# Kernel optimization log

Measured on AMD Instinct MI355X. Metric: run time of the kernel, lower is better.

Reference implementation:

```python
import jax, jax.numpy as jnp
import numpy as np

N_NODES = 200000  # num_users + num_items
N_EDGES = 1000000
D = 64


def setup_inputs() -> dict:
    key = jax.random.key(0)
    ks = jax.random.split(key, 9)
    return {
        "src": jax.random.randint(ks[0], (N_EDGES,), 0, N_NODES, dtype=jnp.int32),
        "dst": jax.random.randint(ks[1], (N_EDGES,), 0, N_NODES, dtype=jnp.int32),
        "review_feat": jax.random.normal(ks[2], (N_EDGES, D), dtype=jnp.float32),
        "ci_r": jax.random.uniform(ks[3], (N_NODES, 1), dtype=jnp.float32),
        "feature": jax.random.normal(ks[4], (N_NODES, D), dtype=jnp.float32),
        "W1": jax.random.normal(ks[5], (D, D), dtype=jnp.float32) * 0.05,
        "W2": jax.random.normal(ks[6], (D, D), dtype=jnp.float32) * 0.05,
        "feature2": jax.random.normal(ks[7], (N_NODES, D), dtype=jnp.float32) * 0.05,
        "feature3": jax.random.normal(ks[8], (N_NODES, D), dtype=jnp.float32) * 0.05,
    }


def reference(src, dst, review_feat, ci_r, feature, W1, W2, feature2, feature3):
    # Eval-mode forward (is_training=False, freeze='', dropout = identity).
    # `feature` is assigned to g.srcdata['h_r'] in the original but never used.
    n = ci_r.shape[0]
    ci_src = ci_r[src]            # [E,1] gather of src norm coeff
    ci_dst = ci_r                 # [N,1]

    # Pass 1: edge linear on review features, scaled by src coeff, scatter-sum.
    r = review_feat @ W1.T                                   # [E,64]
    h1 = jax.ops.segment_sum(r * ci_src, dst, num_segments=n)
    rst_re = h1 * ci_dst

    # Pass 2: (src embedding + edge transform) messages.
    r_fe = review_feat @ W2.T                                # [E,64]
    m2 = (feature2[src] + r_fe) * ci_src
    h2 = jax.ops.segment_sum(m2, dst, num_segments=n)
    rst = h2 * ci_dst

    # Pass 3: pure src-embedding messages.
    m3 = feature3[src] * ci_src
    h3 = jax.ops.segment_sum(m3, dst, num_segments=n)
    rst_id = h3 * ci_dst

    return (rst, rst_re, rst_id)
```

## Files before the change

kernel.cpp:

```cpp
#include <hip/hip_runtime.h>

#define NN 200000
#define NE 1000000
#define DD 64
#define NCHUNK 196

typedef __bf16 bf16x4 __attribute__((ext_vector_type(4)));
typedef __bf16 bf16x8 __attribute__((ext_vector_type(8)));
typedef float  f32x4  __attribute__((ext_vector_type(4)));

static __device__ __forceinline__ bf16x8 pack8(const float* __restrict__ p) {
    float4 a = *reinterpret_cast<const float4*>(p);
    float4 b = *reinterpret_cast<const float4*>(p + 4);
    bf16x8 r;
    r[0] = (__bf16)a.x; r[1] = (__bf16)a.y; r[2] = (__bf16)a.z; r[3] = (__bf16)a.w;
    r[4] = (__bf16)b.x; r[5] = (__bf16)b.y; r[6] = (__bf16)b.z; r[7] = (__bf16)b.w;
    return r;
}

__global__ __launch_bounds__(256) void k_zero(int* __restrict__ counts) {
    const int i = (blockIdx.x * 256 + threadIdx.x) * 4;
    if (i + 3 < NN) *reinterpret_cast<int4*>(counts + i) = make_int4(0, 0, 0, 0);
    else for (int j = i; j < NN; ++j) counts[j] = 0;
}

__global__ __launch_bounds__(256) void k_hist(const int* __restrict__ dst,
                                              int* __restrict__ counts) {
    for (int e = blockIdx.x * blockDim.x + threadIdx.x; e < NE;
         e += gridDim.x * blockDim.x)
        atomicAdd(&counts[dst[e]], 1);
}

__global__ __launch_bounds__(256) void k_chunk_sums(const int* __restrict__ counts,
                                                    int* __restrict__ csum) {
    const int b = blockIdx.x, tid = threadIdx.x;
    const int base = b * 1024 + tid * 4;
    int s = 0;
#pragma unroll
    for (int j = 0; j < 4; ++j) {
        const int i = base + j;
        if (i < NN) s += counts[i];
    }
#pragma unroll
    for (int d = 32; d > 0; d >>= 1) s += __shfl_down(s, d);
    __shared__ int wsum[4];
    if ((tid & 63) == 0) wsum[tid >> 6] = s;
    __syncthreads();
    if (tid == 0) csum[b] = wsum[0] + wsum[1] + wsum[2] + wsum[3];
}

__global__ void k_scan_chunks(const int* __restrict__ csum, int* __restrict__ cofs) {
    if (threadIdx.x == 0 && blockIdx.x == 0) {
        int acc = 0;
        for (int i = 0; i < NCHUNK; ++i) { cofs[i] = acc; acc += csum[i]; }
    }
}

__global__ __launch_bounds__(256) void k_chunk_scan(const int* __restrict__ counts,
                                                    const int* __restrict__ cofs,
                                                    int* __restrict__ offs,
                                                    int* __restrict__ cursor) {
    const int b = blockIdx.x, tid = threadIdx.x;
    const int lane = tid & 63, wv = tid >> 6;
    const int base = b * 1024 + tid * 4;
    int c[4];
#pragma unroll
    for (int j = 0; j < 4; ++j) {
        const int i = base + j;
        c[j] = (i < NN) ? counts[i] : 0;
    }
    const int ls = c[0] + c[1] + c[2] + c[3];
    int v = ls;
#pragma unroll
    for (int d = 1; d < 64; d <<= 1) {
        const int u = __shfl_up(v, d);
        if (lane >= d) v += u;
    }
    __shared__ int wsum[4];
    if (lane == 63) wsum[wv] = v;
    __syncthreads();
    int wbase = 0;
    for (int w = 0; w < wv; ++w) wbase += wsum[w];
    int excl = cofs[b] + wbase + (v - ls);
#pragma unroll
    for (int j = 0; j < 4; ++j) {
        const int i = base + j;
        if (i < NN) { offs[i] = excl; cursor[i] = excl; }
        excl += c[j];
    }
}

__global__ __launch_bounds__(256) void k_permfill(const int* __restrict__ dst,
                                                  const int* __restrict__ src,
                                                  const float* __restrict__ ci,
                                                  int* __restrict__ cursor,
                                                  int4* __restrict__ epack) {
    for (int e = blockIdx.x * blockDim.x + threadIdx.x; e < NE;
         e += gridDim.x * blockDim.x) {
        const int s = src[e];
        const float cs = ci[s];
        const int pos = atomicAdd(&cursor[dst[e]], 1);
        epack[pos] = make_int4(e, s, __float_as_int(cs), 0);
    }
}

__global__ __launch_bounds__(256) void k_pull_fused(
    const int4* __restrict__ epack, const int* __restrict__ offs,
    const int* __restrict__ counts, const float* __restrict__ review,
    const float* __restrict__ ci,
    const float* __restrict__ f2, const float* __restrict__ f3,
    const float* __restrict__ W1, const float* __restrict__ W2,
    float* __restrict__ out_rst, float* __restrict__ out_re,
    float* __restrict__ out_id)
{
    __shared__ __bf16 At[16][72];
    __shared__ float  S2[16][68];

    const int tid = threadIdx.x;
    const int l16 = tid & 15;
    const int q   = tid >> 4;
    const int n   = blockIdx.x * 16 + q;

    const int beg = offs[n];
    const int cnt = counts[n];

    float4 ax0 = {0,0,0,0}, a20 = {0,0,0,0}, a30 = {0,0,0,0};
    float4 ax1 = {0,0,0,0}, a21 = {0,0,0,0}, a31 = {0,0,0,0};

    int k = 0;
    for (; k + 2 <= cnt; k += 2) {
        const int4 ea = epack[beg + k];
        const int4 eb = epack[beg + k + 1];
        const float ca = __int_as_float(ea.z);
        const float cb = __int_as_float(eb.z);
        const float4 ra  = *reinterpret_cast<const float4*>(review + (size_t)ea.x * DD + l16 * 4);
        const float4 rb  = *reinterpret_cast<const float4*>(review + (size_t)eb.x * DD + l16 * 4);
        const float4 p2a = *reinterpret_cast<const float4*>(f2 + (size_t)ea.y * DD + l16 * 4);
        const float4 p2b = *reinterpret_cast<const float4*>(f2 + (size_t)eb.y * DD + l16 * 4);
        const float4 p3a = *reinterpret_cast<const float4*>(f3 + (size_t)ea.y * DD + l16 * 4);
        const float4 p3b = *reinterpret_cast<const float4*>(f3 + (size_t)eb.y * DD + l16 * 4);
        ax0.x = fmaf(ra.x, ca, ax0.x); ax0.y = fmaf(ra.y, ca, ax0.y);
        ax0.z = fmaf(ra.z, ca, ax0.z); ax0.w = fmaf(ra.w, ca, ax0.w);
        ax1.x = fmaf(rb.x, cb, ax1.x); ax1.y = fmaf(rb.y, cb, ax1.y);
        ax1.z = fmaf(rb.z, cb, ax1.z); ax1.w = fmaf(rb.w, cb, ax1.w);
        a20.x = fmaf(p2a.x, ca, a20.x); a20.y = fmaf(p2a.y, ca, a20.y);
        a20.z = fmaf(p2a.z, ca, a20.z); a20.w = fmaf(p2a.w, ca, a20.w);
        a21.x = fmaf(p2b.x, cb, a21.x); a21.y = fmaf(p2b.y, cb, a21.y);
        a21.z = fmaf(p2b.z, cb, a21.z); a21.w = fmaf(p2b.w, cb, a21.w);
        a30.x = fmaf(p3a.x, ca, a30.x); a30.y = fmaf(p3a.y, ca, a30.y);
        a30.z = fmaf(p3a.z, ca, a30.z); a30.w = fmaf(p3a.w, ca, a30.w);
        a31.x = fmaf(p3b.x, cb, a31.x); a31.y = fmaf(p3b.y, cb, a31.y);
        a31.z = fmaf(p3b.z, cb, a31.z); a31.w = fmaf(p3b.w, cb, a31.w);
    }
    if (k < cnt) {
        const int4 ea = epack[beg + k];
        const float ca = __int_as_float(ea.z);
        const float4 ra  = *reinterpret_cast<const float4*>(review + (size_t)ea.x * DD + l16 * 4);
        const float4 p2a = *reinterpret_cast<const float4*>(f2 + (size_t)ea.y * DD + l16 * 4);
        const float4 p3a = *reinterpret_cast<const float4*>(f3 + (size_t)ea.y * DD + l16 * 4);
        ax0.x = fmaf(ra.x, ca, ax0.x); ax0.y = fmaf(ra.y, ca, ax0.y);
        ax0.z = fmaf(ra.z, ca, ax0.z); ax0.w = fmaf(ra.w, ca, ax0.w);
        a20.x = fmaf(p2a.x, ca, a20.x); a20.y = fmaf(p2a.y, ca, a20.y);
        a20.z = fmaf(p2a.z, ca, a20.z); a20.w = fmaf(p2a.w, ca, a20.w);
        a30.x = fmaf(p3a.x, ca, a30.x); a30.y = fmaf(p3a.y, ca, a30.y);
        a30.z = fmaf(p3a.z, ca, a30.z); a30.w = fmaf(p3a.w, ca, a30.w);
    }

    const float cid = ci[n];
    float4 ax = {ax0.x + ax1.x, ax0.y + ax1.y, ax0.z + ax1.z, ax0.w + ax1.w};
    float4 a2 = {a20.x + a21.x, a20.y + a21.y, a20.z + a21.z, a20.w + a21.w};
    float4 a3 = {a30.x + a31.x, a30.y + a31.y, a30.z + a31.z, a30.w + a31.w};

    f32x4 v3 = {a3.x * cid, a3.y * cid, a3.z * cid, a3.w * cid};
    __builtin_nontemporal_store(v3, reinterpret_cast<f32x4*>(out_id + (size_t)n * DD + l16 * 4));

    bf16x4 hb;
    hb[0] = (__bf16)(ax.x * cid); hb[1] = (__bf16)(ax.y * cid);
    hb[2] = (__bf16)(ax.z * cid); hb[3] = (__bf16)(ax.w * cid);
    *reinterpret_cast<bf16x4*>(&At[q][l16 * 4]) = hb;
    float4 s2v = {a2.x * cid, a2.y * cid, a2.z * cid, a2.w * cid};
    *reinterpret_cast<float4*>(&S2[q][l16 * 4]) = s2v;
    __syncthreads();

    const int w  = tid >> 6;
    const int lq = (tid & 63) >> 4;
    bf16x8 w1f[2], w2f[2];
#pragma unroll
    for (int kk = 0; kk < 2; ++kk) {
        const int off = (w * 16 + l16) * DD + kk * 32 + lq * 8;
        w1f[kk] = pack8(W1 + off);
        w2f[kk] = pack8(W2 + off);
    }
    const bf16x8 a0 = *reinterpret_cast<const bf16x8*>(&At[l16][lq * 8]);
    const bf16x8 a1 = *reinterpret_cast<const bf16x8*>(&At[l16][lq * 8 + 32]);

    const f32x4 zero = {0.f, 0.f, 0.f, 0.f};
    f32x4 acc1 = zero, acc2 = zero;
    acc1 = __builtin_amdgcn_mfma_f32_16x16x32_bf16(a0, w1f[0], acc1, 0, 0, 0);
    acc1 = __builtin_amdgcn_mfma_f32_16x16x32_bf16(a1, w1f[1], acc1, 0, 0, 0);
    acc2 = __builtin_amdgcn_mfma_f32_16x16x32_bf16(a0, w2f[0], acc2, 0, 0, 0);
    acc2 = __builtin_amdgcn_mfma_f32_16x16x32_bf16(a1, w2f[1], acc2, 0, 0, 0);

    const int base = blockIdx.x * 16;
#pragma unroll
    for (int i = 0; i < 4; ++i) {
        const int row = lq * 4 + i;
        const size_t o = (size_t)(base + row) * DD + w * 16 + l16;
        __builtin_nontemporal_store(acc1[i], out_re + o);
        __builtin_nontemporal_store(acc2[i] + S2[row][w * 16 + l16], out_rst + o);
    }
}

__global__ __launch_bounds__(256) void gcn_mfma_kernel(
    const int* __restrict__ src, const int* __restrict__ dst,
    const float* __restrict__ review, const float* __restrict__ ci,
    const float* __restrict__ W1, const float* __restrict__ W2,
    const float* __restrict__ f2, const float* __restrict__ f3,
    float* __restrict__ out)
{
    float* out_rst = out;
    float* out_re  = out + (size_t)NN * DD;
    float* out_id  = out + 2 * (size_t)NN * DD;
    const int lane = threadIdx.x & 63;
    const int l16  = lane & 15;
    const int lq   = lane >> 4;
    const int wid  = blockIdx.x * (blockDim.x >> 6) + (threadIdx.x >> 6);
    const int nw   = gridDim.x * (blockDim.x >> 6);

    bf16x8 w1f[4][2], w2f[4][2];
#pragma unroll
    for (int c = 0; c < 4; ++c)
#pragma unroll
        for (int kk = 0; kk < 2; ++kk) {
            const int off = (c * 16 + l16) * DD + kk * 32 + lq * 8;
            w1f[c][kk] = pack8(W1 + off);
            w2f[c][kk] = pack8(W2 + off);
        }
    const f32x4 zero = {0.f, 0.f, 0.f, 0.f};
    for (int t = wid; t < NE / 16; t += nw) {
        const int e0 = t * 16;
        const float* xr = review + (size_t)(e0 + l16) * DD + lq * 8;
        const bf16x8 a0 = pack8(xr);
        const bf16x8 a1 = pack8(xr + 32);
        f32x4 acc1[4], acc2[4];
#pragma unroll
        for (int c = 0; c < 4; ++c) { acc1[c] = zero; acc2[c] = zero; }
#pragma unroll
        for (int c = 0; c < 4; ++c) {
            acc1[c] = __builtin_amdgcn_mfma_f32_16x16x32_bf16(a0, w1f[c][0], acc1[c], 0, 0, 0);
            acc1[c] = __builtin_amdgcn_mfma_f32_16x16x32_bf16(a1, w1f[c][1], acc1[c], 0, 0, 0);
            acc2[c] = __builtin_amdgcn_mfma_f32_16x16x32_bf16(a0, w2f[c][0], acc2[c], 0, 0, 0);
            acc2[c] = __builtin_amdgcn_mfma_f32_16x16x32_bf16(a1, w2f[c][1], acc2[c], 0, 0, 0);
        }
        int sA[4], dA[4]; float cf[4];
#pragma unroll
        for (int i = 0; i < 4; ++i) {
            const int e = e0 + lq * 4 + i;
            sA[i] = src[e]; dA[i] = dst[e];
            cf[i] = ci[sA[i]] * ci[dA[i]];
        }
#pragma unroll
        for (int i = 0; i < 4; ++i) {
            const size_t so = (size_t)sA[i] * DD;
            const size_t dofs = (size_t)dA[i] * DD;
            const float c_ = cf[i];
#pragma unroll
            for (int c = 0; c < 4; ++c) {
                const int col = c * 16 + l16;
                atomicAdd(out_re  + dofs + col, acc1[c][i] * c_);
                atomicAdd(out_rst + dofs + col, (f2[so + col] + acc2[c][i]) * c_);
                atomicAdd(out_id  + dofs + col, f3[so + col] * c_);
            }
        }
    }
}

extern "C" void kernel_launch(void* const* d_in, const int* in_sizes, int n_in,
                              void* d_out, int out_size, void* d_ws, size_t ws_size,
                              hipStream_t stream) {
    const int*   src    = (const int*)d_in[0];
    const int*   dst    = (const int*)d_in[1];
    const float* review = (const float*)d_in[2];
    const float* ci     = (const float*)d_in[3];
    const float* W1     = (const float*)d_in[5];
    const float* W2     = (const float*)d_in[6];
    const float* f2     = (const float*)d_in[7];
    const float* f3     = (const float*)d_in[8];
    float* out = (float*)d_out;
    float* out_rst = out;
    float* out_re  = out + (size_t)NN * DD;
    float* out_id  = out + 2 * (size_t)NN * DD;

    const size_t NEED = sizeof(int) * ((size_t)3 * NN + 512) +
                        sizeof(int4) * (size_t)NE;
    if (ws_size < NEED) {
        (void)hipMemsetAsync(out, 0, (size_t)out_size * sizeof(float), stream);
        gcn_mfma_kernel<<<2048, 256, 0, stream>>>(src, dst, review, ci, W1, W2, f2, f3, out);
        return;
    }

    char* w = (char*)d_ws;
    int* counts = (int*)w;    w += (size_t)NN * 4;
    int* offs   = (int*)w;    w += (size_t)NN * 4;
    int* cursor = (int*)w;    w += (size_t)NN * 4;
    int* csum   = (int*)w;    w += 256 * 4;
    int* cofs   = (int*)w;    w += 256 * 4;
    int4* epack = (int4*)w;

    k_zero        <<<(NN / 4 + 255) / 256, 256, 0, stream>>>(counts);
    k_hist        <<<1024, 256, 0, stream>>>(dst, counts);
    k_chunk_sums  <<<NCHUNK, 256, 0, stream>>>(counts, csum);
    k_scan_chunks <<<1, 64, 0, stream>>>(csum, cofs);
    k_chunk_scan  <<<NCHUNK, 256, 0, stream>>>(counts, cofs, offs, cursor);
    k_permfill    <<<1024, 256, 0, stream>>>(dst, src, ci, cursor, epack);
    k_pull_fused  <<<NN / 16, 256, 0, stream>>>(epack, offs, counts, review, ci,
                                                f2, f3, W1, W2,
                                                out_rst, out_re, out_id);
}
```

Before: 295.8 us.

## Pre-scale feature2/feature3 into packed bf16 table and pull per-wave node groups

Adds a conversion pass, co-scheduled with the edge permutation fill in one launch, that writes feature2 and feature3 pre-multiplied by ci as one interleaved bf16 row per node. The pull kernel then gathers a single 256-byte bf16 row per edge instead of two fp32 rows, roughly halving gather traffic for those tables. It also reorganises work so each 16-lane group walks a contiguous CSR range of 4 nodes, using offs[n+1] instead of counts, and each wave runs its own MFMA projection without a block barrier. The cost is the extra conversion pass, added workspace, and bf16 rounding of the src features and of the pass-2/3 messages, plus serial per-edge loads with only one-edge prefetch.

```diff
diff --git a/kernel.cpp b/kernel.cpp
--- a/kernel.cpp
+++ b/kernel.cpp
@@ -63,6 +63,7 @@
     const int b = blockIdx.x, tid = threadIdx.x;
     const int lane = tid & 63, wv = tid >> 6;
     const int base = b * 1024 + tid * 4;
+    if (b == 0 && tid == 0) offs[NN] = NE;
     int c[4];
 #pragma unroll
     for (int j = 0; j < 4; ++j) {
@@ -90,124 +91,131 @@
     }
 }
 
-__global__ __launch_bounds__(256) void k_permfill(const int* __restrict__ dst,
-                                                  const int* __restrict__ src,
-                                                  const float* __restrict__ ci,
-                                                  int* __restrict__ cursor,
-                                                  int4* __restrict__ epack) {
-    for (int e = blockIdx.x * blockDim.x + threadIdx.x; e < NE;
-         e += gridDim.x * blockDim.x) {
-        const int s = src[e];
-        const float cs = ci[s];
-        const int pos = atomicAdd(&cursor[dst[e]], 1);
-        epack[pos] = make_int4(e, s, __float_as_int(cs), 0);
-    }
-}
-
-__global__ __launch_bounds__(256) void k_pull_fused(
+__global__ __launch_bounds__(256) void k_fill_conv(
+    const int* __restrict__ dst, const int* __restrict__ src,
+    const float* __restrict__ ci, const float* __restrict__ f2,
+    const float* __restrict__ f3, int* __restrict__ cursor,
+    int4* __restrict__ epack, __bf16* __restrict__ ftc)
+{
+    const int b = blockIdx.x;
+    if (b < 1024) {
+        for (int e = b * 256 + threadIdx.x; e < NE; e += 1024 * 256) {
+            const int s = src[e];
+            const float cs = ci[s];
+            const int pos = atomicAdd(&cursor[dst[e]], 1);
+            epack[pos] = make_int4(e, s, __float_as_int(cs), 0);
+        }
+    } else {
+        const int nconv = (gridDim.x - 1024) * 256;
+        const int total = NN * 16;
+        for (int cch = (b - 1024) * 256 + threadIdx.x; cch < total; cch += nconv) {
+            const int row = cch >> 4;
+            const int t   = cch & 15;
+            const float c = ci[row];
+            const float4 a = *reinterpret_cast<const float4*>(f2 + (size_t)row * DD + t * 4);
+            const float4 v = *reinterpret_cast<const float4*>(f3 + (size_t)row * DD + t * 4);
+            bf16x8 o;
+            o[0] = (__bf16)(a.x * c); o[1] = (__bf16)(a.y * c);
+            o[2] = (__bf16)(a.z * c); o[3] = (__bf16)(a.w * c);
+            o[4] = (__bf16)(v.x * c); o[5] = (__bf16)(v.y * c);
+            o[6] = (__bf16)(v.z * c); o[7] = (__bf16)(v.w * c);
+            *reinterpret_cast<bf16x8*>(ftc + (size_t)row * 128 + t * 8) = o;
+        }
+    }
+}
+
+__global__ __launch_bounds__(256) void k_pull_ws(
     const int4* __restrict__ epack, const int* __restrict__ offs,
-    const int* __restrict__ counts, const float* __restrict__ review,
-    const float* __restrict__ ci,
-    const float* __restrict__ f2, const float* __restrict__ f3,
+    const float* __restrict__ review, const float* __restrict__ ci,
+    const __bf16* __restrict__ ftc,
     const float* __restrict__ W1, const float* __restrict__ W2,
     float* __restrict__ out_rst, float* __restrict__ out_re,
     float* __restrict__ out_id)
 {
-    __shared__ __bf16 At[16][72];
-    __shared__ float  S2[16][68];
-
-    const int tid = threadIdx.x;
-    const int l16 = tid & 15;
-    const int q   = tid >> 4;
-    const int n   = blockIdx.x * 16 + q;
-
-    const int beg = offs[n];
-    const int cnt = counts[n];
-
-    float4 ax0 = {0,0,0,0}, a20 = {0,0,0,0}, a30 = {0,0,0,0};
-    float4 ax1 = {0,0,0,0}, a21 = {0,0,0,0}, a31 = {0,0,0,0};
-
-    int k = 0;
-    for (; k + 2 <= cnt; k += 2) {
-        const int4 ea = epack[beg + k];
-        const int4 eb = epack[beg + k + 1];
-        const float ca = __int_as_float(ea.z);
-        const float cb = __int_as_float(eb.z);
-        const float4 ra  = *reinterpret_cast<const float4*>(review + (size_t)ea.x * DD + l16 * 4);
-        const float4 rb  = *reinterpret_cast<const float4*>(review + (size_t)eb.x * DD + l16 * 4);
-        const float4 p2a = *reinterpret_cast<const float4*>(f2 + (size_t)ea.y * DD + l16 * 4);
-        const float4 p2b = *reinterpret_cast<const float4*>(f2 + (size_t)eb.y * DD + l16 * 4);
-        const float4 p3a = *reinterpret_cast<const float4*>(f3 + (size_t)ea.y * DD + l16 * 4);
-        const float4 p3b = *reinterpret_cast<const float4*>(f3 + (size_t)eb.y * DD + l16 * 4);
-        ax0.x = fmaf(ra.x, ca, ax0.x); ax0.y = fmaf(ra.y, ca, ax0.y);
-        ax0.z = fmaf(ra.z, ca, ax0.z); ax0.w = fmaf(ra.w, ca, ax0.w);
-        ax1.x = fmaf(rb.x, cb, ax1.x); ax1.y = fmaf(rb.y, cb, ax1.y);
-        ax1.z = fmaf(rb.z, cb, ax1.z); ax1.w = fmaf(rb.w, cb, ax1.w);
-        a20.x = fmaf(p2a.x, ca, a20.x); a20.y = fmaf(p2a.y, ca, a20.y);
-        a20.z = fmaf(p2a.z, ca, a20.z); a20.w = fmaf(p2a.w, ca, a20.w);
-        a21.x = fmaf(p2b.x, cb, a21.x); a21.y = fmaf(p2b.y, cb, a21.y);
-        a21.z = fmaf(p2b.z, cb, a21.z); a21.w = fmaf(p2b.w, cb, a21.w);
-        a30.x = fmaf(p3a.x, ca, a30.x); a30.y = fmaf(p3a.y, ca, a30.y);
-        a30.z = fmaf(p3a.z, ca, a30.z); a30.w = fmaf(p3a.w, ca, a30.w);
-        a31.x = fmaf(p3b.x, cb, a31.x); a31.y = fmaf(p3b.y, cb, a31.y);
-        a31.z = fmaf(p3b.z, cb, a31.z); a31.w = fmaf(p3b.w, cb, a31.w);
-    }
-    if (k < cnt) {
-        const int4 ea = epack[beg + k];
-        const float ca = __int_as_float(ea.z);
-        const float4 ra  = *reinterpret_cast<const float4*>(review + (size_t)ea.x * DD + l16 * 4);
-        const float4 p2a = *reinterpret_cast<const float4*>(f2 + (size_t)ea.y * DD + l16 * 4);
-        const float4 p3a = *reinterpret_cast<const float4*>(f3 + (size_t)ea.y * DD + l16 * 4);
-        ax0.x = fmaf(ra.x, ca, ax0.x); ax0.y = fmaf(ra.y, ca, ax0.y);
-        ax0.z = fmaf(ra.z, ca, ax0.z); ax0.w = fmaf(ra.w, ca, ax0.w);
-        a20.x = fmaf(p2a.x, ca, a20.x); a20.y = fmaf(p2a.y, ca, a20.y);
-        a20.z = fmaf(p2a.z, ca, a20.z); a20.w = fmaf(p2a.w, ca, a20.w);
-        a30.x = fmaf(p3a.x, ca, a30.x); a30.y = fmaf(p3a.y, ca, a30.y);
-        a30.z = fmaf(p3a.z, ca, a30.z); a30.w = fmaf(p3a.w, ca, a30.w);
-    }
-
-    const float cid = ci[n];
-    float4 ax = {ax0.x + ax1.x, ax0.y + ax1.y, ax0.z + ax1.z, ax0.w + ax1.w};
-    float4 a2 = {a20.x + a21.x, a20.y + a21.y, a20.z + a21.z, a20.w + a21.w};
-    float4 a3 = {a30.x + a31.x, a30.y + a31.y, a30.z + a31.z, a30.w + a31.w};
-
-    f32x4 v3 = {a3.x * cid, a3.y * cid, a3.z * cid, a3.w * cid};
-    __builtin_nontemporal_store(v3, reinterpret_cast<f32x4*>(out_id + (size_t)n * DD + l16 * 4));
-
-    bf16x4 hb;
-    hb[0] = (__bf16)(ax.x * cid); hb[1] = (__bf16)(ax.y * cid);
-    hb[2] = (__bf16)(ax.z * cid); hb[3] = (__bf16)(ax.w * cid);
-    *reinterpret_cast<bf16x4*>(&At[q][l16 * 4]) = hb;
-    float4 s2v = {a2.x * cid, a2.y * cid, a2.z * cid, a2.w * cid};
-    *reinterpret_cast<float4*>(&S2[q][l16 * 4]) = s2v;
-    __syncthreads();
-
-    const int w  = tid >> 6;
-    const int lq = (tid & 63) >> 4;
-    bf16x8 w1f[2], w2f[2];
-#pragma unroll
-    for (int kk = 0; kk < 2; ++kk) {
-        const int off = (w * 16 + l16) * DD + kk * 32 + lq * 8;
-        w1f[kk] = pack8(W1 + off);
-        w2f[kk] = pack8(W2 + off);
-    }
-    const bf16x8 a0 = *reinterpret_cast<const bf16x8*>(&At[l16][lq * 8]);
-    const bf16x8 a1 = *reinterpret_cast<const bf16x8*>(&At[l16][lq * 8 + 32]);
+    __shared__ __bf16 At[4][16][72];
+    __shared__ float  S2[4][16][68];
+
+    const int tid   = threadIdx.x;
+    const int w     = tid >> 6;
+    const int lane  = tid & 63;
+    const int l16   = lane & 15;
+    const int q     = lane >> 4;
+    const int wbase = blockIdx.x * 64 + w * 16;
+    const int n0q   = wbase + q * 4;
+
+    int pos = offs[n0q];
+    const int posEnd = offs[n0q + 4];
+    int j   = 0;
+    int bnd = offs[n0q + 1];
+
+    float4 ax = make_float4(0.f, 0.f, 0.f, 0.f);
+    float4 a2 = make_float4(0.f, 0.f, 0.f, 0.f);
+    float4 a3 = make_float4(0.f, 0.f, 0.f, 0.f);
+
+    int4 ep = epack[pos < posEnd ? pos : (NE - 1)];
+
+    for (;;) {
+        while (j < 4 && pos == bnd) {
+            const int n = n0q + j;
+            const float cid = ci[n];
+            f32x4 v3 = {a3.x * cid, a3.y * cid, a3.z * cid, a3.w * cid};
+            __builtin_nontemporal_store(
+                v3, reinterpret_cast<f32x4*>(out_id + (size_t)n * DD + l16 * 4));
+            bf16x4 hb;
+            hb[0] = (__bf16)(ax.x * cid); hb[1] = (__bf16)(ax.y * cid);
+            hb[2] = (__bf16)(ax.z * cid); hb[3] = (__bf16)(ax.w * cid);
+            *reinterpret_cast<bf16x4*>(&At[w][q * 4 + j][l16 * 4]) = hb;
+            f32x4 s2v = {a2.x * cid, a2.y * cid, a2.z * cid, a2.w * cid};
+            *reinterpret_cast<f32x4*>(&S2[w][q * 4 + j][l16 * 4]) = s2v;
+            ax = make_float4(0.f, 0.f, 0.f, 0.f);
+            a2 = make_float4(0.f, 0.f, 0.f, 0.f);
+            a3 = make_float4(0.f, 0.f, 0.f, 0.f);
+            ++j;
+            bnd = (j < 4) ? offs[n0q + j + 1] : 0x7fffffff;
+        }
+        if (j == 4) break;
+
+        const float cs = __int_as_float(ep.z);
+        const float4 r = *reinterpret_cast<const float4*>(
+            review + (size_t)ep.x * DD + l16 * 4);
+        const bf16x8 t = *reinterpret_cast<const bf16x8*>(
+            ftc + (size_t)ep.y * 128 + l16 * 8);
+        ++pos;
+        ep = epack[pos < posEnd ? pos : (NE - 1)];
+
+        ax.x = fmaf(r.x, cs, ax.x); ax.y = fmaf(r.y, cs, ax.y);
+        ax.z = fmaf(r.z, cs, ax.z); ax.w = fmaf(r.w, cs, ax.w);
+        a2.x += (float)t[0]; a2.y += (float)t[1];
+        a2.z += (float)t[2]; a2.w += (float)t[3];
+        a3.x += (float)t[4]; a3.y += (float)t[5];
+        a3.z += (float)t[6]; a3.w += (float)t[7];
+    }
+
+    asm volatile("s_waitcnt lgkmcnt(0)" ::: "memory");
+
+    const bf16x8 a0 = *reinterpret_cast<const bf16x8*>(&At[w][l16][q * 8]);
+    const bf16x8 a1 = *reinterpret_cast<const bf16x8*>(&At[w][l16][q * 8 + 32]);
 
     const f32x4 zero = {0.f, 0.f, 0.f, 0.f};
-    f32x4 acc1 = zero, acc2 = zero;
-    acc1 = __builtin_amdgcn_mfma_f32_16x16x32_bf16(a0, w1f[0], acc1, 0, 0, 0);
-    acc1 = __builtin_amdgcn_mfma_f32_16x16x32_bf16(a1, w1f[1], acc1, 0, 0, 0);
-    acc2 = __builtin_amdgcn_mfma_f32_16x16x32_bf16(a0, w2f[0], acc2, 0, 0, 0);
-    acc2 = __builtin_amdgcn_mfma_f32_16x16x32_bf16(a1, w2f[1], acc2, 0, 0, 0);
-
-    const int base = blockIdx.x * 16;
-#pragma unroll
-    for (int i = 0; i < 4; ++i) {
-        const int row = lq * 4 + i;
-        const size_t o = (size_t)(base + row) * DD + w * 16 + l16;
-        __builtin_nontemporal_store(acc1[i], out_re + o);
-        __builtin_nontemporal_store(acc2[i] + S2[row][w * 16 + l16], out_rst + o);
+#pragma unroll
+    for (int c = 0; c < 4; ++c) {
+        const int off = (c * 16 + l16) * DD + q * 8;
+        const bf16x8 w1f0 = pack8(W1 + off);
+        const bf16x8 w1f1 = pack8(W1 + off + 32);
+        const bf16x8 w2f0 = pack8(W2 + off);
+        const bf16x8 w2f1 = pack8(W2 + off + 32);
+        f32x4 acc1 = zero, acc2 = zero;
+        acc1 = __builtin_amdgcn_mfma_f32_16x16x32_bf16(a0, w1f0, acc1, 0, 0, 0);
+        acc1 = __builtin_amdgcn_mfma_f32_16x16x32_bf16(a1, w1f1, acc1, 0, 0, 0);
+        acc2 = __builtin_amdgcn_mfma_f32_16x16x32_bf16(a0, w2f0, acc2, 0, 0, 0);
+        acc2 = __builtin_amdgcn_mfma_f32_16x16x32_bf16(a1, w2f1, acc2, 0, 0, 0);
+#pragma unroll
+        for (int i = 0; i < 4; ++i) {
+            const int row = q * 4 + i;
+            const size_t o = (size_t)(wbase + row) * DD + c * 16 + l16;
+            __builtin_nontemporal_store(acc1[i], out_re + o);
+            __builtin_nontemporal_store(acc2[i] + S2[w][row][c * 16 + l16], out_rst + o);
+        }
     }
 }
 
@@ -291,8 +299,9 @@
     float* out_re  = out + (size_t)NN * DD;
     float* out_id  = out + 2 * (size_t)NN * DD;
 
-    const size_t NEED = sizeof(int) * ((size_t)3 * NN + 512) +
-                        sizeof(int4) * (size_t)NE;
+    const size_t NEED = sizeof(int) * ((size_t)3 * NN + 1 + 512) +
+                        sizeof(int4) * (size_t)NE +
+                        sizeof(__bf16) * (size_t)NN * 128;
     if (ws_size < NEED) {
         (void)hipMemsetAsync(out, 0, (size_t)out_size * sizeof(float), stream);
         gcn_mfma_kernel<<<2048, 256, 0, stream>>>(src, dst, review, ci, W1, W2, f2, f3, out);
@@ -301,19 +310,19 @@
 
     char* w = (char*)d_ws;
     int* counts = (int*)w;    w += (size_t)NN * 4;
-    int* offs   = (int*)w;    w += (size_t)NN * 4;
+    int* offs   = (int*)w;    w += ((size_t)NN + 1) * 4;
     int* cursor = (int*)w;    w += (size_t)NN * 4;
     int* csum   = (int*)w;    w += 256 * 4;
     int* cofs   = (int*)w;    w += 256 * 4;
-    int4* epack = (int4*)w;
-
-    k_zero        <<<(NN / 4 + 255) / 256, 256, 0, stream>>>(counts);
-    k_hist        <<<1024, 256, 0, stream>>>(dst, counts);
-    k_chunk_sums  <<<NCHUNK, 256, 0, stream>>>(counts, csum);
-    k_scan_chunks <<<1, 64, 0, stream>>>(csum, cofs);
-    k_chunk_scan  <<<NCHUNK, 256, 0, stream>>>(counts, cofs, offs, cursor);
-    k_permfill    <<<1024, 256, 0, stream>>>(dst, src, ci, cursor, epack);
-    k_pull_fused  <<<NN / 16, 256, 0, stream>>>(epack, offs, counts, review, ci,
-                                                f2, f3, W1, W2,
-                                                out_rst, out_re, out_id);
-}
+    int4* epack = (int4*)w;   w += (size_t)NE * 16;
+    __bf16* ftc = (__bf16*)w;
+
+    k_zero       <<<(NN / 4 + 255) / 256, 256, 0, stream>>>(counts);
+    k_hist       <<<1024, 256, 0, stream>>>(dst, counts);
+    k_chunk_sums <<<NCHUNK, 256, 0, stream>>>(counts, csum);
+    k_scan_chunks<<<1, 64, 0, stream>>>(csum, cofs);
+    k_chunk_scan <<<NCHUNK, 256, 0, stream>>>(counts, cofs, offs, cursor);
+    k_fill_conv  <<<3072, 256, 0, stream>>>(dst, src, ci, f2, f3, cursor, epack, ftc);
+    k_pull_ws    <<<NN / 64, 256, 0, stream>>>(epack, offs, review, ci, ftc,
+                                               W1, W2, out_rst, out_re, out_id);
+}
```

After: 342.0 us. +15.6%, slower.

## Pre-scale and pack feature2/feature3 into bf16 interleaved table for gather

Applied to the files above, without the earlier changes.

Adds a prep pass, fused with the histogram kernel, that multiplies feature2 and feature3 rows by ci and stores them interleaved as bf16 in one 256-byte row per node. The pull kernel then does a single 16-byte gather per edge for both tables instead of two 16-byte fp32 gathers, roughly halving random-gather traffic for passes 2 and 3. The edge loop is also unrolled to 4 with independent accumulators and nontemporal loads for epack and review. This trades an extra streaming conversion pass and bf16 rounding of the messages for less gather bandwidth.

```diff
diff --git a/kernel.cpp b/kernel.cpp
--- a/kernel.cpp
+++ b/kernel.cpp
@@ -8,6 +8,7 @@
 typedef __bf16 bf16x4 __attribute__((ext_vector_type(4)));
 typedef __bf16 bf16x8 __attribute__((ext_vector_type(8)));
 typedef float  f32x4  __attribute__((ext_vector_type(4)));
+typedef int    i32x4  __attribute__((ext_vector_type(4)));
 
 static __device__ __forceinline__ bf16x8 pack8(const float* __restrict__ p) {
     float4 a = *reinterpret_cast<const float4*>(p);
@@ -24,11 +25,32 @@
     else for (int j = i; j < NN; ++j) counts[j] = 0;
 }
 
-__global__ __launch_bounds__(256) void k_hist(const int* __restrict__ dst,
-                                              int* __restrict__ counts) {
-    for (int e = blockIdx.x * blockDim.x + threadIdx.x; e < NE;
-         e += gridDim.x * blockDim.x)
-        atomicAdd(&counts[dst[e]], 1);
+__global__ __launch_bounds__(256) void k_prep(
+    const int* __restrict__ dst, const float* __restrict__ f2,
+    const float* __restrict__ f3, const float* __restrict__ ci,
+    int* __restrict__ counts, __bf16* __restrict__ ftc)
+{
+    const int b = blockIdx.x;
+    if (b < 1024) {
+        for (int e = b * 256 + threadIdx.x; e < NE; e += 1024 * 256)
+            atomicAdd(&counts[dst[e]], 1);
+    } else {
+        const int nconv = (gridDim.x - 1024) * 256;
+        const int total = NN * 16;
+        for (int cch = (b - 1024) * 256 + threadIdx.x; cch < total; cch += nconv) {
+            const int row = cch >> 4;
+            const int t   = cch & 15;
+            const float c = ci[row];
+            const float4 a = *reinterpret_cast<const float4*>(f2 + (size_t)row * DD + t * 4);
+            const float4 v = *reinterpret_cast<const float4*>(f3 + (size_t)row * DD + t * 4);
+            bf16x8 o;
+            o[0] = (__bf16)(a.x * c); o[1] = (__bf16)(a.y * c);
+            o[2] = (__bf16)(a.z * c); o[3] = (__bf16)(a.w * c);
+            o[4] = (__bf16)(v.x * c); o[5] = (__bf16)(v.y * c);
+            o[6] = (__bf16)(v.z * c); o[7] = (__bf16)(v.w * c);
+            *reinterpret_cast<bf16x8*>(ftc + (size_t)row * 128 + t * 8) = o;
+        }
+    }
 }
 
 __global__ __launch_bounds__(256) void k_chunk_sums(const int* __restrict__ counts,
@@ -107,8 +129,7 @@
 __global__ __launch_bounds__(256) void k_pull_fused(
     const int4* __restrict__ epack, const int* __restrict__ offs,
     const int* __restrict__ counts, const float* __restrict__ review,
-    const float* __restrict__ ci,
-    const float* __restrict__ f2, const float* __restrict__ f3,
+    const float* __restrict__ ci, const __bf16* __restrict__ ftc,
     const float* __restrict__ W1, const float* __restrict__ W2,
     float* __restrict__ out_rst, float* __restrict__ out_re,
     float* __restrict__ out_id)
@@ -124,62 +145,79 @@
     const int beg = offs[n];
     const int cnt = counts[n];
 
-    float4 ax0 = {0,0,0,0}, a20 = {0,0,0,0}, a30 = {0,0,0,0};
-    float4 ax1 = {0,0,0,0}, a21 = {0,0,0,0}, a31 = {0,0,0,0};
+    f32x4 ax[4], a2[4], a3[4];
+#pragma unroll
+    for (int u = 0; u < 4; ++u) {
+        ax[u] = (f32x4){0.f, 0.f, 0.f, 0.f};
+        a2[u] = (f32x4){0.f, 0.f, 0.f, 0.f};
+        a3[u] = (f32x4){0.f, 0.f, 0.f, 0.f};
+    }
 
     int k = 0;
-    for (; k + 2 <= cnt; k += 2) {
-        const int4 ea = epack[beg + k];
-        const int4 eb = epack[beg + k + 1];
-        const float ca = __int_as_float(ea.z);
-        const float cb = __int_as_float(eb.z);
-        const float4 ra  = *reinterpret_cast<const float4*>(review + (size_t)ea.x * DD + l16 * 4);
-        const float4 rb  = *reinterpret_cast<const float4*>(review + (size_t)eb.x * DD + l16 * 4);
-        const float4 p2a = *reinterpret_cast<const float4*>(f2 + (size_t)ea.y * DD + l16 * 4);
-        const float4 p2b = *reinterpret_cast<const float4*>(f2 + (size_t)eb.y * DD + l16 * 4);
-        const float4 p3a = *reinterpret_cast<const float4*>(f3 + (size_t)ea.y * DD + l16 * 4);
-        const float4 p3b = *reinterpret_cast<const float4*>(f3 + (size_t)eb.y * DD + l16 * 4);
-        ax0.x = fmaf(ra.x, ca, ax0.x); ax0.y = fmaf(ra.y, ca, ax0.y);
-        ax0.z = fmaf(ra.z, ca, ax0.z); ax0.w = fmaf(ra.w, ca, ax0.w);
-        ax1.x = fmaf(rb.x, cb, ax1.x); ax1.y = fmaf(rb.y, cb, ax1.y);
-        ax1.z = fmaf(rb.z, cb, ax1.z); ax1.w = fmaf(rb.w, cb, ax1.w);
-        a20.x = fmaf(p2a.x, ca, a20.x); a20.y = fmaf(p2a.y, ca, a20.y);
-        a20.z = fmaf(p2a.z, ca, a20.z); a20.w = fmaf(p2a.w, ca, a20.w);
-        a21.x = fmaf(p2b.x, cb, a21.x); a21.y = fmaf(p2b.y, cb, a21.y);
-        a21.z = fmaf(p2b.z, cb, a21.z); a21.w = fmaf(p2b.w, cb, a21.w);
-        a30.x = fmaf(p3a.x, ca, a30.x); a30.y = fmaf(p3a.y, ca, a30.y);
-        a30.z = fmaf(p3a.z, ca, a30.z); a30.w = fmaf(p3a.w, ca, a30.w);
-        a31.x = fmaf(p3b.x, cb, a31.x); a31.y = fmaf(p3b.y, cb, a31.y);
-        a31.z = fmaf(p3b.z, cb, a31.z); a31.w = fmaf(p3b.w, cb, a31.w);
-    }
-    if (k < cnt) {
-        const int4 ea = epack[beg + k];
-        const float ca = __int_as_float(ea.z);
-        const float4 ra  = *reinterpret_cast<const float4*>(review + (size_t)ea.x * DD + l16 * 4);
-        const float4 p2a = *reinterpret_cast<const float4*>(f2 + (size_t)ea.y * DD + l16 * 4);
-        const float4 p3a = *reinterpret_cast<const float4*>(f3 + (size_t)ea.y * DD + l16 * 4);
-        ax0.x = fmaf(ra.x, ca, ax0.x); ax0.y = fmaf(ra.y, ca, ax0.y);
-        ax0.z = fmaf(ra.z, ca, ax0.z); ax0.w = fmaf(ra.w, ca, ax0.w);
-        a20.x = fmaf(p2a.x, ca, a20.x); a20.y = fmaf(p2a.y, ca, a20.y);
-        a20.z = fmaf(p2a.z, ca, a20.z); a20.w = fmaf(p2a.w, ca, a20.w);
-        a30.x = fmaf(p3a.x, ca, a30.x); a30.y = fmaf(p3a.y, ca, a30.y);
-        a30.z = fmaf(p3a.z, ca, a30.z); a30.w = fmaf(p3a.w, ca, a30.w);
+    for (; k + 4 <= cnt; k += 4) {
+        i32x4 ep[4];
+#pragma unroll
+        for (int u = 0; u < 4; ++u)
+            ep[u] = __builtin_nontemporal_load(
+                reinterpret_cast<const i32x4*>(epack + (size_t)(beg + k + u)));
+        f32x4 r[4];
+        bf16x8 t[4];
+#pragma unroll
+        for (int u = 0; u < 4; ++u) {
+            r[u] = __builtin_nontemporal_load(reinterpret_cast<const f32x4*>(
+                review + (size_t)ep[u][0] * DD + l16 * 4));
+            t[u] = *reinterpret_cast<const bf16x8*>(
+                ftc + (size_t)ep[u][1] * 128 + l16 * 8);
+        }
+#pragma unroll
+        for (int u = 0; u < 4; ++u) {
+            const float cs = __int_as_float(ep[u][2]);
+            ax[u][0] = fmaf(r[u][0], cs, ax[u][0]);
+            ax[u][1] = fmaf(r[u][1], cs, ax[u][1]);
+            ax[u][2] = fmaf(r[u][2], cs, ax[u][2]);
+            ax[u][3] = fmaf(r[u][3], cs, ax[u][3]);
+            a2[u][0] += (float)t[u][0]; a2[u][1] += (float)t[u][1];
+            a2[u][2] += (float)t[u][2]; a2[u][3] += (float)t[u][3];
+            a3[u][0] += (float)t[u][4]; a3[u][1] += (float)t[u][5];
+            a3[u][2] += (float)t[u][6]; a3[u][3] += (float)t[u][7];
+        }
+    }
+    for (; k < cnt; ++k) {
+        const int u = k & 3;
+        const i32x4 ep = __builtin_nontemporal_load(
+            reinterpret_cast<const i32x4*>(epack + (size_t)(beg + k)));
+        const f32x4 r = __builtin_nontemporal_load(reinterpret_cast<const f32x4*>(
+            review + (size_t)ep[0] * DD + l16 * 4));
+        const bf16x8 t = *reinterpret_cast<const bf16x8*>(
+            ftc + (size_t)ep[1] * 128 + l16 * 8);
+        const float cs = __int_as_float(ep[2]);
+        ax[u][0] = fmaf(r[0], cs, ax[u][0]);
+        ax[u][1] = fmaf(r[1], cs, ax[u][1]);
+        ax[u][2] = fmaf(r[2], cs, ax[u][2]);
+        ax[u][3] = fmaf(r[3], cs, ax[u][3]);
+        a2[u][0] += (float)t[0]; a2[u][1] += (float)t[1];
+        a2[u][2] += (float)t[2]; a2[u][3] += (float)t[3];
+        a3[u][0] += (float)t[4]; a3[u][1] += (float)t[5];
+        a3[u][2] += (float)t[6]; a3[u][3] += (float)t[7];
     }
 
     const float cid = ci[n];
-    float4 ax = {ax0.x + ax1.x, ax0.y + ax1.y, ax0.z + ax1.z, ax0.w + ax1.w};
-    float4 a2 = {a20.x + a21.x, a20.y + a21.y, a20.z + a21.z, a20.w + a21.w};
-    float4 a3 = {a30.x + a31.x, a30.y + a31.y, a30.z + a31.z, a30.w + a31.w};
-
-    f32x4 v3 = {a3.x * cid, a3.y * cid, a3.z * cid, a3.w * cid};
+    f32x4 axs = {ax[0][0]+ax[1][0]+ax[2][0]+ax[3][0], ax[0][1]+ax[1][1]+ax[2][1]+ax[3][1],
+                 ax[0][2]+ax[1][2]+ax[2][2]+ax[3][2], ax[0][3]+ax[1][3]+ax[2][3]+ax[3][3]};
+    f32x4 a2s = {a2[0][0]+a2[1][0]+a2[2][0]+a2[3][0], a2[0][1]+a2[1][1]+a2[2][1]+a2[3][1],
+                 a2[0][2]+a2[1][2]+a2[2][2]+a2[3][2], a2[0][3]+a2[1][3]+a2[2][3]+a2[3][3]};
+    f32x4 a3s = {a3[0][0]+a3[1][0]+a3[2][0]+a3[3][0], a3[0][1]+a3[1][1]+a3[2][1]+a3[3][1],
+                 a3[0][2]+a3[1][2]+a3[2][2]+a3[3][2], a3[0][3]+a3[1][3]+a3[2][3]+a3[3][3]};
+
+    f32x4 v3 = {a3s[0] * cid, a3s[1] * cid, a3s[2] * cid, a3s[3] * cid};
     __builtin_nontemporal_store(v3, reinterpret_cast<f32x4*>(out_id + (size_t)n * DD + l16 * 4));
 
     bf16x4 hb;
-    hb[0] = (__bf16)(ax.x * cid); hb[1] = (__bf16)(ax.y * cid);
-    hb[2] = (__bf16)(ax.z * cid); hb[3] = (__bf16)(ax.w * cid);
+    hb[0] = (__bf16)(axs[0] * cid); hb[1] = (__bf16)(axs[1] * cid);
+    hb[2] = (__bf16)(axs[2] * cid); hb[3] = (__bf16)(axs[3] * cid);
     *reinterpret_cast<bf16x4*>(&At[q][l16 * 4]) = hb;
-    float4 s2v = {a2.x * cid, a2.y * cid, a2.z * cid, a2.w * cid};
-    *reinterpret_cast<float4*>(&S2[q][l16 * 4]) = s2v;
+    f32x4 s2v = {a2s[0] * cid, a2s[1] * cid, a2s[2] * cid, a2s[3] * cid};
+    *reinterpret_cast<f32x4*>(&S2[q][l16 * 4]) = s2v;
     __syncthreads();
 
     const int w  = tid >> 6;
@@ -292,7 +330,8 @@
     float* out_id  = out + 2 * (size_t)NN * DD;
 
     const size_t NEED = sizeof(int) * ((size_t)3 * NN + 512) +
-                        sizeof(int4) * (size_t)NE;
+                        sizeof(int4) * (size_t)NE +
+                        sizeof(__bf16) * (size_t)NN * 128;
     if (ws_size < NEED) {
         (void)hipMemsetAsync(out, 0, (size_t)out_size * sizeof(float), stream);
         gcn_mfma_kernel<<<2048, 256, 0, stream>>>(src, dst, review, ci, W1, W2, f2, f3, out);
@@ -305,15 +344,15 @@
     int* cursor = (int*)w;    w += (size_t)NN * 4;
     int* csum   = (int*)w;    w += 256 * 4;
     int* cofs   = (int*)w;    w += 256 * 4;
-    int4* epack = (int4*)w;
-
-    k_zero        <<<(NN / 4 + 255) / 256, 256, 0, stream>>>(counts);
-    k_hist        <<<1024, 256, 0, stream>>>(dst, counts);
-    k_chunk_sums  <<<NCHUNK, 256, 0, stream>>>(counts, csum);
-    k_scan_chunks <<<1, 64, 0, stream>>>(csum, cofs);
-    k_chunk_scan  <<<NCHUNK, 256, 0, stream>>>(counts, cofs, offs, cursor);
-    k_permfill    <<<1024, 256, 0, stream>>>(dst, src, ci, cursor, epack);
-    k_pull_fused  <<<NN / 16, 256, 0, stream>>>(epack, offs, counts, review, ci,
-                                                f2, f3, W1, W2,
-                                                out_rst, out_re, out_id);
-}
+    int4* epack = (int4*)w;   w += (size_t)NE * 16;
+    __bf16* ftc = (__bf16*)w;
+
+    k_zero       <<<(NN / 4 + 255) / 256, 256, 0, stream>>>(counts);
+    k_prep       <<<3072, 256, 0, stream>>>(dst, f2, f3, ci, counts, ftc);
+    k_chunk_sums <<<NCHUNK, 256, 0, stream>>>(counts, csum);
+    k_scan_chunks<<<1, 64, 0, stream>>>(csum, cofs);
+    k_chunk_scan <<<NCHUNK, 256, 0, stream>>>(counts, cofs, offs, cursor);
+    k_permfill   <<<1024, 256, 0, stream>>>(dst, src, ci, cursor, epack);
+    k_pull_fused <<<NN / 16, 256, 0, stream>>>(epack, offs, counts, review, ci, ftc,
+                                               W1, W2, out_rst, out_re, out_id);
+}
```

New measurement: 424.0 us. +43.3%, slower.
